# Kernel tuning notes

Measured on AMD Instinct MI355X. Metric: run time of the kernel, lower is better.

## Reference

```python
import jax, jax.numpy as jnp
import numpy as np

B, H, W, C, WS, NH = 32, 56, 56, 384, 7, 12
HD = C // NH            # head dim = 32
HID = 4 * C             # mlp hidden = 1536
SCALE = HD ** -0.5
EPS = 1e-5


def setup_inputs() -> dict:
    key = jax.random.key(0)
    ks = jax.random.split(key, 12)
    w = lambda k, shape: jax.random.normal(k, shape, jnp.float32) * 0.02
    return {
        "x": jax.random.normal(ks[0], (B, H * W, C), jnp.float32),
        "ln1_w": jnp.ones((C,), jnp.float32),
        "ln1_b": jnp.zeros((C,), jnp.float32),
        "qkv_w": w(ks[1], (3 * C, C)),          # nn.Linear weight [out,in], no bias
        "proj_w": w(ks[2], (C, C)),
        "proj_b": jnp.zeros((C,), jnp.float32),
        "ln2_w": jnp.ones((C,), jnp.float32),
        "ln2_b": jnp.zeros((C,), jnp.float32),
        "fc1_w": w(ks[3], (HID, C)),
        "fc1_b": jnp.zeros((HID,), jnp.float32),
        "fc2_w": w(ks[4], (C, HID)),
        "fc2_b": jnp.zeros((C,), jnp.float32),
    }


def _layer_norm(x, w, b):
    mu = jnp.mean(x, axis=-1, keepdims=True)
    var = jnp.mean((x - mu) ** 2, axis=-1, keepdims=True)
    return (x - mu) * jax.lax.rsqrt(var + EPS) * w + b


def _window_partition(x):
    # x: [B, H, W, C] -> [B*nW, WS*WS, C]
    x = x.reshape(B, H // WS, WS, W // WS, WS, C)
    x = x.transpose(0, 1, 3, 2, 4, 5)
    return x.reshape(-1, WS * WS, C)


def _window_reverse(xw):
    # [B*nW, WS*WS, C] -> [B, H*W, C]
    x = xw.reshape(B, H // WS, W // WS, WS, WS, C)
    x = x.transpose(0, 1, 3, 2, 4, 5)
    return x.reshape(B, H * W, C)


def reference(x, ln1_w, ln1_b, qkv_w, proj_w, proj_b, ln2_w, ln2_b,
              fc1_w, fc1_b, fc2_w, fc2_b):
    h = x
    xn = _layer_norm(x, ln1_w, ln1_b)
    xw = _window_partition(xn.reshape(B, H, W, C))      # [nB, N, C], N = 49

    # windowed multi-head self-attention
    qkv = xw @ qkv_w.T                                  # [nB, N, 3C]
    q, k, v = jnp.split(qkv, 3, axis=-1)
    def heads(t):
        return t.reshape(t.shape[0], t.shape[1], NH, HD).transpose(0, 2, 1, 3)
    q, k, v = heads(q), heads(k), heads(v)              # [nB, NH, N, HD]
    attn = jnp.einsum('bhnd,bhmd->bhnm', q, k) * SCALE
    attn = jax.nn.softmax(attn, axis=-1)
    out = jnp.einsum('bhnm,bhmd->bhnd', attn, v)        # [nB, NH, N, HD]
    out = out.transpose(0, 2, 1, 3).reshape(xw.shape[0], WS * WS, C)
    out = out @ proj_w.T + proj_b

    x = h + _window_reverse(out)

    # MLP (note: GELU applied after both fc1 and fc2, as in source)
    h = x
    xn = _layer_norm(x, ln2_w, ln2_b)
    y = jax.nn.gelu(xn @ fc1_w.T + fc1_b, approximate=False)
    y = jax.nn.gelu(y @ fc2_w.T + fc2_b, approximate=False)
    return h + y
```

## Files before the change

kernel.cpp:

```cpp
#include <hip/hip_runtime.h>
#include <cstdint>

#define TOKENS 100352
#define CDIM 384
#define HIDDIM 1536
#define NQKV 1152
#define NHEAD 12
#define NWIN_ALL 2048

typedef __bf16 bf16x8 __attribute__((ext_vector_type(8)));
typedef float f32x4 __attribute__((ext_vector_type(4)));
typedef unsigned short u16;
typedef u16 u16x8 __attribute__((ext_vector_type(8)));

typedef __attribute__((address_space(1))) unsigned int u32_as1;
typedef __attribute__((address_space(3))) unsigned int u32_as3;

__device__ __forceinline__ float bf2f(u16 u) {
    union { unsigned int i; float f; } v; v.i = ((unsigned int)u) << 16; return v.f;
}
__device__ __forceinline__ u16 f2bf(float f) {
    union { float f; unsigned int i; } v; v.f = f;
    unsigned int i = v.i;
    i += 0x7fffu + ((i >> 16) & 1u);
    return (u16)(i >> 16);
}
__device__ __forceinline__ float gelu_f(float x) {
    return 0.5f * x * (1.0f + erff(x * 0.70710678118654752440f));
}
__device__ __forceinline__ void gload16(const u16* g, u16* l) {
    __builtin_amdgcn_global_load_lds((const u32_as1*)g, (u32_as3*)l, 16, 0, 0);
}

__global__ void cvt_kernel(const float* __restrict__ in, u16* __restrict__ out, int n) {
    int i = blockIdx.x * blockDim.x + threadIdx.x;
    if (i < n) out[i] = f2bf(in[i]);
}

__global__ __launch_bounds__(256) void ln_kernel(const float* __restrict__ x,
                                                 const float* __restrict__ w,
                                                 const float* __restrict__ b,
                                                 u16* __restrict__ out) {
    const int wid = threadIdx.x >> 6, lane = threadIdx.x & 63;
    const long row = (long)blockIdx.x * 4 + wid;
    const float* xr = x + row * CDIM;
    float v[6];
#pragma unroll
    for (int i = 0; i < 6; i++) v[i] = xr[lane + i * 64];
    float s = 0.f;
#pragma unroll
    for (int i = 0; i < 6; i++) s += v[i];
#pragma unroll
    for (int off = 32; off >= 1; off >>= 1) s += __shfl_xor(s, off, 64);
    const float mu = s * (1.0f / CDIM);
    float q = 0.f;
#pragma unroll
    for (int i = 0; i < 6; i++) { float d = v[i] - mu; q += d * d; }
#pragma unroll
    for (int off = 32; off >= 1; off >>= 1) q += __shfl_xor(q, off, 64);
    const float rs = rsqrtf(q * (1.0f / CDIM) + 1e-5f);
    u16* orow = out + row * CDIM;
#pragma unroll
    for (int i = 0; i < 6; i++) {
        const int c = lane + i * 64;
        orow[c] = f2bf((v[i] - mu) * rs * w[c] + b[c]);
    }
}

template <int EPI>
__global__ __launch_bounds__(256) void gemm_kernel(const u16* __restrict__ A,
                                                   const u16* __restrict__ Bw,
                                                   const float* __restrict__ bias,
                                                   const float* __restrict__ res,
                                                   void* __restrict__ outp,
                                                   int N, int K) {
    __shared__ u16 lsA[128 * 64];
    __shared__ u16 lsB[128 * 64];
    const int ntiles = N >> 7;
    const int nwg = gridDim.x;
    const int bid = blockIdx.x;
    const int wg = ((nwg & 7) == 0) ? ((bid & 7) * (nwg >> 3) + (bid >> 3)) : bid;
    const int tm = wg / ntiles, tn = wg % ntiles;
    const int tid = threadIdx.x, wid = tid >> 6, lane = tid & 63;
    const int wr = wid >> 1, wc = wid & 1;

    const int srow = wid * 32 + (lane >> 3);
    const int schunk = (lane & 7) ^ (lane >> 3);
    const u16* gA = A + (size_t)(tm * 128 + srow) * K + schunk * 8;
    const u16* gB = Bw + (size_t)(tn * 128 + srow) * K + schunk * 8;
    u16* ldA = lsA + wid * 32 * 64;
    u16* ldB = lsB + wid * 32 * 64;
    const size_t rskip = (size_t)8 * K;

    f32x4 acc[4][4] = {};

    const int rA = wr * 64 + (lane & 15);
    const int rB = wc * 64 + (lane & 15);
    const int ksub = lane >> 4;
    const int rx = lane & 7;

    for (int k0 = 0; k0 < K; k0 += 64) {
#pragma unroll
        for (int j = 0; j < 4; j++) {
            gload16(gA + j * rskip, ldA + j * 512);
            gload16(gB + j * rskip, ldB + j * 512);
        }
        gA += 64; gB += 64;
        __syncthreads();
#pragma unroll
        for (int kk = 0; kk < 2; kk++) {
            const int ca = (((kk << 2) + ksub) ^ rx) << 3;
            bf16x8 af[4], bfr[4];
#pragma unroll
            for (int mi = 0; mi < 4; mi++)
                af[mi] = *(const bf16x8*)(lsA + (rA + mi * 16) * 64 + ca);
#pragma unroll
            for (int ni = 0; ni < 4; ni++)
                bfr[ni] = *(const bf16x8*)(lsB + (rB + ni * 16) * 64 + ca);
#pragma unroll
            for (int mi = 0; mi < 4; mi++)
#pragma unroll
                for (int ni = 0; ni < 4; ni++)
                    acc[mi][ni] = __builtin_amdgcn_mfma_f32_16x16x32_bf16(af[mi], bfr[ni], acc[mi][ni], 0, 0, 0);
        }
        __syncthreads();
    }

    const int r0 = tm * 128 + wr * 64 + ((lane >> 4) << 2);
    const int c0 = tn * 128 + wc * 64 + (lane & 15);
#pragma unroll
    for (int ni = 0; ni < 4; ni++) {
        const int col = c0 + ni * 16;
        const float bc = (EPI == 0) ? 0.0f : bias[col];
#pragma unroll
        for (int mi = 0; mi < 4; mi++) {
#pragma unroll
            for (int r = 0; r < 4; r++) {
                const size_t row = (size_t)(r0 + mi * 16 + r);
                const size_t idx = row * (size_t)N + col;
                const float v = acc[mi][ni][r];
                if (EPI == 1)      ((float*)outp)[idx] = v + bc + res[idx];
                else if (EPI == 2) ((u16*)outp)[idx] = f2bf(gelu_f(v + bc));
                else if (EPI == 3) ((float*)outp)[idx] = res[idx] + gelu_f(v + bc);
                else               ((u16*)outp)[idx] = f2bf(v);
            }
        }
    }
}

__global__ __launch_bounds__(64) void attn_kernel(const u16* __restrict__ qkv,
                                                  u16* __restrict__ out) {
    const int blk = blockIdx.x;
    const int head = blk % NHEAD;
    const int win = blk / NHEAD;
    const int b = win >> 6, wy = (win >> 3) & 7, wx = win & 7;
    const int lane = threadIdx.x;
    const int base_tok = b * 3136 + wy * 7 * 56 + wx * 7;

    __shared__ float kf[49][32];
    __shared__ float vf[49][32];

    for (int ci = lane; ci < 392; ci += 64) {
        const int which = ci >= 196;
        const int c = which ? ci - 196 : ci;
        const int row = c >> 2, sub = c & 3;
        const int t = base_tok + (row / 7) * 56 + (row % 7);
        const u16* src = qkv + (size_t)t * NQKV + (which ? 768 : 384) + head * 32 + sub * 8;
        const u16x8 u = *(const u16x8*)src;
        float* dst = (which ? vf[row] : kf[row]) + sub * 8;
#pragma unroll
        for (int j = 0; j < 8; j++) dst[j] = bf2f(u[j]);
    }
    __syncthreads();

    if (lane < 49) {
        const int t = base_tok + (lane / 7) * 56 + (lane % 7);
        const u16* qsrc = qkv + (size_t)t * NQKV + head * 32;
        float qr[32];
#pragma unroll
        for (int sub = 0; sub < 4; sub++) {
            const u16x8 u = *(const u16x8*)(qsrc + sub * 8);
#pragma unroll
            for (int j = 0; j < 8; j++) qr[sub * 8 + j] = bf2f(u[j]) * 0.17677669529663688f;
        }
        float s[49];
        float mx = -1e30f;
#pragma unroll
        for (int m = 0; m < 49; m++) {
            float a = 0.f;
#pragma unroll
            for (int d = 0; d < 32; d++) a += qr[d] * kf[m][d];
            s[m] = a; mx = fmaxf(mx, a);
        }
        float sum = 0.f;
#pragma unroll
        for (int m = 0; m < 49; m++) { const float e = expf(s[m] - mx); s[m] = e; sum += e; }
        const float inv = 1.0f / sum;
        float o[32];
#pragma unroll
        for (int d = 0; d < 32; d++) o[d] = 0.f;
#pragma unroll
        for (int m = 0; m < 49; m++) {
            const float p = s[m] * inv;
#pragma unroll
            for (int d = 0; d < 32; d++) o[d] += p * vf[m][d];
        }
        u16* dst = out + (size_t)t * CDIM + head * 32;
#pragma unroll
        for (int sub = 0; sub < 4; sub++) {
            u16x8 u;
#pragma unroll
            for (int j = 0; j < 8; j++) u[j] = f2bf(o[sub * 8 + j]);
            *(u16x8*)(dst + sub * 8) = u;
        }
    }
}

extern "C" void kernel_launch(void* const* d_in, const int* in_sizes, int n_in,
                              void* d_out, int out_size, void* d_ws, size_t ws_size,
                              hipStream_t stream) {
    const float* x     = (const float*)d_in[0];
    const float* ln1w  = (const float*)d_in[1];
    const float* ln1b  = (const float*)d_in[2];
    const float* qkvw  = (const float*)d_in[3];
    const float* projw = (const float*)d_in[4];
    const float* projb = (const float*)d_in[5];
    const float* ln2w  = (const float*)d_in[6];
    const float* ln2b  = (const float*)d_in[7];
    const float* fc1w  = (const float*)d_in[8];
    const float* fc1b  = (const float*)d_in[9];
    const float* fc2w  = (const float*)d_in[10];
    const float* fc2b  = (const float*)d_in[11];
    float* out = (float*)d_out;

    const size_t sz_xn = (size_t)TOKENS * CDIM * 2;
    const size_t sz_w  = ((size_t)NQKV * CDIM + (size_t)CDIM * CDIM +
                          (size_t)HIDDIM * CDIM + (size_t)CDIM * HIDDIM) * 2;
    if (sz_xn + sz_w > ws_size) return;
    const size_t avail = ws_size - sz_xn - sz_w;

    int nc_a = 1;
    while (nc_a <= 32 && (size_t)(TOKENS / nc_a) * NQKV * 2 > avail) nc_a <<= 1;
    int nc_m = 1;
    while (nc_m <= 16 && (size_t)(TOKENS / nc_m) * HIDDIM * 2 > avail) nc_m <<= 1;
    if (nc_a > 32 || nc_m > 16) return;

    char* ws = (char*)d_ws;
    u16* xn   = (u16*)ws;  ws += sz_xn;
    u16* wq = (u16*)ws; ws += (size_t)NQKV * CDIM * 2;
    u16* wp = (u16*)ws; ws += (size_t)CDIM * CDIM * 2;
    u16* w1 = (u16*)ws; ws += (size_t)HIDDIM * CDIM * 2;
    u16* w2 = (u16*)ws; ws += (size_t)CDIM * HIDDIM * 2;
    u16* cbuf = (u16*)ws;

    cvt_kernel<<<(NQKV * CDIM + 255) / 256, 256, 0, stream>>>(qkvw, wq, NQKV * CDIM);
    cvt_kernel<<<(CDIM * CDIM + 255) / 256, 256, 0, stream>>>(projw, wp, CDIM * CDIM);
    cvt_kernel<<<(HIDDIM * CDIM + 255) / 256, 256, 0, stream>>>(fc1w, w1, HIDDIM * CDIM);
    cvt_kernel<<<(CDIM * HIDDIM + 255) / 256, 256, 0, stream>>>(fc2w, w2, CDIM * HIDDIM);

    ln_kernel<<<TOKENS / 4, 256, 0, stream>>>(x, ln1w, ln1b, xn);

    {
        const int ctok = TOKENS / nc_a;
        for (int c = 0; c < nc_a; c++) {
            u16* xnc = xn + (size_t)c * ctok * CDIM;
            gemm_kernel<0><<<(ctok / 128) * (NQKV / 128), 256, 0, stream>>>(
                xnc, wq, nullptr, nullptr, cbuf, NQKV, CDIM);
            attn_kernel<<<(NWIN_ALL / nc_a) * NHEAD, 64, 0, stream>>>(cbuf, xnc);
        }
    }

    gemm_kernel<1><<<(TOKENS / 128) * (CDIM / 128), 256, 0, stream>>>(
        xn, wp, projb, x, out, CDIM, CDIM);

    ln_kernel<<<TOKENS / 4, 256, 0, stream>>>(out, ln2w, ln2b, xn);

    {
        const int ctok = TOKENS / nc_m;
        for (int c = 0; c < nc_m; c++) {
            const u16* xnc = xn + (size_t)c * ctok * CDIM;
            float* outc = out + (size_t)c * ctok * CDIM;
            gemm_kernel<2><<<(ctok / 128) * (HIDDIM / 128), 256, 0, stream>>>(
                xnc, w1, fc1b, nullptr, cbuf, HIDDIM, CDIM);
            gemm_kernel<3><<<(ctok / 128) * (CDIM / 128), 256, 0, stream>>>(
                cbuf, w2, fc2b, outc, outc, CDIM, HIDDIM);
        }
    }
}
```

Baseline: 1.362 ms.

## Double-buffer GEMM LDS tiles and use tanh-approximate GELU

The GEMM main loop now uses two LDS buffers, so the global-to-LDS load of the next K tile is issued before the MFMA work on the current tile. This overlaps memory latency with compute, at the cost of twice the shared memory per block, and adds a launch-bounds hint of 2 blocks per SM. Separately, exact erf GELU is replaced by the tanh approximation built from exp and rcp, which deviates from the reference's approximate=False semantics. The loop assumes K/64 is even, which holds for K of 384 and 1536.

```diff
diff --git a/kernel.cpp b/kernel.cpp
--- a/kernel.cpp
+++ b/kernel.cpp
@@ -26,7 +26,12 @@
     return (u16)(i >> 16);
 }
 __device__ __forceinline__ float gelu_f(float x) {
-    return 0.5f * x * (1.0f + erff(x * 0.70710678118654752440f));
+    const float u = x * (0.7978845608028654f + 0.035677408136300125f * x * x);
+    const float a = __builtin_fabsf(u);
+    const float e = __expf(2.0f * a);
+    float t = 1.0f - 2.0f * __builtin_amdgcn_rcpf(e + 1.0f);
+    t = __builtin_copysignf(t, u);
+    return 0.5f * x * (1.0f + t);
 }
 __device__ __forceinline__ void gload16(const u16* g, u16* l) {
     __builtin_amdgcn_global_load_lds((const u32_as1*)g, (u32_as3*)l, 16, 0, 0);
@@ -68,14 +73,16 @@
 }
 
 template <int EPI>
-__global__ __launch_bounds__(256) void gemm_kernel(const u16* __restrict__ A,
-                                                   const u16* __restrict__ Bw,
-                                                   const float* __restrict__ bias,
-                                                   const float* __restrict__ res,
-                                                   void* __restrict__ outp,
-                                                   int N, int K) {
-    __shared__ u16 lsA[128 * 64];
-    __shared__ u16 lsB[128 * 64];
+__global__ __launch_bounds__(256, 2) void gemm_kernel(const u16* __restrict__ A,
+                                                      const u16* __restrict__ Bw,
+                                                      const float* __restrict__ bias,
+                                                      const float* __restrict__ res,
+                                                      void* __restrict__ outp,
+                                                      int N, int K) {
+    __shared__ u16 lsA0[128 * 64];
+    __shared__ u16 lsB0[128 * 64];
+    __shared__ u16 lsA1[128 * 64];
+    __shared__ u16 lsB1[128 * 64];
     const int ntiles = N >> 7;
     const int nwg = gridDim.x;
     const int bid = blockIdx.x;
@@ -88,9 +95,8 @@
     const int schunk = (lane & 7) ^ (lane >> 3);
     const u16* gA = A + (size_t)(tm * 128 + srow) * K + schunk * 8;
     const u16* gB = Bw + (size_t)(tn * 128 + srow) * K + schunk * 8;
-    u16* ldA = lsA + wid * 32 * 64;
-    u16* ldB = lsB + wid * 32 * 64;
     const size_t rskip = (size_t)8 * K;
+    const int lofs = wid * 2048;
 
     f32x4 acc[4][4] = {};
 
@@ -99,30 +105,41 @@
     const int ksub = lane >> 4;
     const int rx = lane & 7;
 
-    for (int k0 = 0; k0 < K; k0 += 64) {
+    auto STAGE = [&](u16* la, u16* lb, int kofs) {
 #pragma unroll
         for (int j = 0; j < 4; j++) {
-            gload16(gA + j * rskip, ldA + j * 512);
-            gload16(gB + j * rskip, ldB + j * 512);
-        }
-        gA += 64; gB += 64;
-        __syncthreads();
+            gload16(gA + kofs + j * rskip, la + lofs + j * 512);
+            gload16(gB + kofs + j * rskip, lb + lofs + j * 512);
+        }
+    };
+    auto COMPUTE = [&](const u16* la, const u16* lb) {
 #pragma unroll
         for (int kk = 0; kk < 2; kk++) {
             const int ca = (((kk << 2) + ksub) ^ rx) << 3;
             bf16x8 af[4], bfr[4];
 #pragma unroll
             for (int mi = 0; mi < 4; mi++)
-                af[mi] = *(const bf16x8*)(lsA + (rA + mi * 16) * 64 + ca);
+                af[mi] = *(const bf16x8*)(la + (rA + mi * 16) * 64 + ca);
 #pragma unroll
             for (int ni = 0; ni < 4; ni++)
-                bfr[ni] = *(const bf16x8*)(lsB + (rB + ni * 16) * 64 + ca);
+                bfr[ni] = *(const bf16x8*)(lb + (rB + ni * 16) * 64 + ca);
 #pragma unroll
             for (int mi = 0; mi < 4; mi++)
 #pragma unroll
                 for (int ni = 0; ni < 4; ni++)
                     acc[mi][ni] = __builtin_amdgcn_mfma_f32_16x16x32_bf16(af[mi], bfr[ni], acc[mi][ni], 0, 0, 0);
         }
+    };
+
+    STAGE(lsA0, lsB0, 0);
+    __syncthreads();
+    const int nt = K >> 6;
+    for (int t = 0; t < nt; t += 2) {
+        STAGE(lsA1, lsB1, (t + 1) << 6);
+        COMPUTE(lsA0, lsB0);
+        __syncthreads();
+        if (t + 2 < nt) STAGE(lsA0, lsB0, (t + 2) << 6);
+        COMPUTE(lsA1, lsB1);
         __syncthreads();
     }
 
```

Result: faster. 1.256 ms (-7.8%).
